# Performance work log

Hardware: AMD Instinct MI355X
Metric: run time of the kernel (lower is better)

Reference implementation:

```python
import jax, jax.numpy as jnp
import numpy as np
from jax import lax

HEADS = 8
DIM_HEAD = 64
INNER = HEADS * DIM_HEAD  # 512
LOG_SCALE_MAX = float(np.log(100.0))  # clamp for clamp_exp (SwinV2-style max temperature 1/0.01)
EPS_NORM = 1e-12  # F.normalize eps
EPS_LN = 1e-5


def setup_inputs() -> dict:
    key = jax.random.key(0)
    ks = jax.random.split(key, 6)
    b, c, h, w = 2, 256, 48, 48
    x = jax.random.normal(ks[0], (b, c, h, w), jnp.float32)
    w_in = jax.random.normal(ks[1], (3 * INNER, c), jnp.float32) * (c ** -0.5)
    b_in = jnp.zeros((3 * INNER,), jnp.float32)
    # learnable log-scale, init log(d_head ** -0.5), per head
    softmax_scale = jnp.full((HEADS, 1, 1), float(np.log(DIM_HEAD ** -0.5)), jnp.float32)
    w_dw = jax.random.normal(ks[2], (INNER, 1, 3, 3), jnp.float32) * (1.0 / 3.0)
    w_pw = jax.random.normal(ks[3], (2 * c, INNER), jnp.float32) * (INNER ** -0.5)
    gamma = jnp.full((2 * c,), 1e-3, jnp.float32)  # norm init_weight=0.001
    beta = jnp.zeros((2 * c,), jnp.float32)
    return {"x": x, "w_in": w_in, "b_in": b_in, "softmax_scale": softmax_scale,
            "w_dw": w_dw, "w_pw": w_pw, "gamma": gamma, "beta": beta}


def _l2norm(t):
    n = jnp.sqrt(jnp.sum(t * t, axis=-1, keepdims=True))
    return t / jnp.maximum(n, EPS_NORM)


def reference(x, w_in, b_in, softmax_scale, w_dw, w_pw, gamma, beta):
    b, c, h, w = x.shape
    s = h * w
    # proj_in: 1x1 conv then 'b (h c) x y -> b h x y c'
    y = jnp.einsum('bchw,oc->bohw', x, w_in) + b_in[None, :, None, None]
    y = y.reshape(b, HEADS, 3 * DIM_HEAD, h, w).transpose(0, 1, 3, 4, 2)  # b H x y (3*dh)
    y = y.reshape(b, HEADS, s, 3 * DIM_HEAD)
    q, k, v = jnp.split(y, 3, axis=-1)  # each [b, H, s, dh]
    # scaled cosine attention
    qn, kn = _l2norm(q), _l2norm(k)
    scale = jnp.exp(jnp.minimum(softmax_scale, LOG_SCALE_MAX))  # clamp_exp, [H,1,1]
    sim = jnp.einsum('bhid,bhjd->bhij', qn, kn) * scale[None]
    attn = jax.nn.softmax(sim, axis=-1)
    out = jnp.einsum('bhij,bhjd->bhid', attn, v)  # [b,H,s,dh]
    # unsplit heads -> 'b (h w) c' -> 'b c h w'
    update = out.transpose(0, 2, 1, 3).reshape(b, s, INNER)
    update = update.transpose(0, 2, 1).reshape(b, INNER, h, w)
    # proj_out: depthwise 3x3 (no bias) + pointwise 1x1 (no bias)
    dw = lax.conv_general_dilated(update, w_dw, (1, 1), 'SAME',
                                  feature_group_count=INNER,
                                  dimension_numbers=('NCHW', 'OIHW', 'NCHW'))
    pw = jnp.einsum('bchw,oc->bohw', dw, w_pw)  # [b, 2c, h, w]
    # channelwise layernorm with small init weight (norm_scales_and_shifts)
    mu = jnp.mean(pw, axis=1, keepdims=True)
    var = jnp.var(pw, axis=1, keepdims=True)
    normed = (pw - mu) * lax.rsqrt(var + EPS_LN)
    normed = normed * gamma[None, :, None, None] + beta[None, :, None, None]
    scales, shifts = jnp.split(normed, 2, axis=1)  # each [b, c, h, w]
    return shifts + x * scales
```

## Files before the change

### kernel.cpp

```cpp
#include <hip/hip_runtime.h>

#define B_ 2
#define C_ 256
#define S_ 2304
#define DH_ 64
#define O3_ 1536
#define INNER_ 512
#define LOGSMAX 4.605170185988092f
#define LOG2E 1.4426950408889634f

typedef __attribute__((ext_vector_type(8))) short short8;
typedef __attribute__((ext_vector_type(4))) float f32x4;
typedef __attribute__((ext_vector_type(16))) float f32x16;
typedef __attribute__((ext_vector_type(4))) unsigned short us4;
typedef __attribute__((ext_vector_type(2))) unsigned u32x2;
typedef __attribute__((ext_vector_type(4))) unsigned u32x4;
typedef __bf16 bf16x8 __attribute__((ext_vector_type(8)));

__device__ __forceinline__ unsigned short f2bf(float f) {
  unsigned u = __builtin_bit_cast(unsigned, f);
  u += 0x7FFFu + ((u >> 16) & 1u);
  return (unsigned short)(u >> 16);
}
__device__ __forceinline__ float bf2f(unsigned short h) {
  return __builtin_bit_cast(float, (unsigned)h << 16);
}
__device__ __forceinline__ bf16x8 as_bf(short8 v) {
  return __builtin_bit_cast(bf16x8, v);
}
__device__ __forceinline__ float fexp2(float x) {
#if __has_builtin(__builtin_amdgcn_exp2f)
  return __builtin_amdgcn_exp2f(x);
#else
  return __expf(x * 0.6931471805599453f);
#endif
}
__device__ __forceinline__ float frcp(float x) {
#if __has_builtin(__builtin_amdgcn_rcpf)
  return __builtin_amdgcn_rcpf(x);
#else
  return 1.f / x;
#endif
}
__device__ __forceinline__ unsigned pack_hi16(unsigned b, unsigned a) {
  return __builtin_amdgcn_perm(b, a, 0x07060302u);
}
__device__ __forceinline__ unsigned pack_lo16(unsigned b, unsigned a) {
  return __builtin_amdgcn_perm(b, a, 0x05040100u);
}

__global__ __launch_bounds__(256) void k_prep(const float* __restrict__ x,
                                              const float* __restrict__ w_in,
                                              const float* __restrict__ w_pw,
                                              unsigned short* __restrict__ xT,
                                              unsigned short* __restrict__ w_inb,
                                              unsigned short* __restrict__ w_pwb) {
  __shared__ float tile[64][65];
  int blk = blockIdx.x;
  int t = threadIdx.x;
  if (blk < 288) {
    int p0 = (blk % 36) * 64, c0 = ((blk / 36) % 4) * 64, b = blk / 144;
    const float* xb = x + (size_t)b * C_ * S_;
#pragma unroll
    for (int i = 0; i < 16; i++) {
      int c = i * 4 + (t >> 6);
      int p = t & 63;
      tile[c][p] = xb[(size_t)(c0 + c) * S_ + p0 + p];
    }
    __syncthreads();
    unsigned short* xTb = xT + (size_t)b * S_ * C_;
#pragma unroll
    for (int i = 0; i < 16; i++) {
      int p = i * 4 + (t >> 6);
      int c = t & 63;
      xTb[(size_t)(p0 + p) * C_ + c0 + c] = f2bf(tile[c][p]);
    }
  } else if (blk < 288 + 1536) {
    int i = (blk - 288) * 256 + t;
    w_inb[i] = f2bf(w_in[i]);
  } else {
    int i = (blk - 1824) * 256 + t;
    w_pwb[i] = f2bf(w_pw[i]);
  }
}

__global__ __launch_bounds__(256) void k_gemm_qkv(const unsigned short* __restrict__ A,
                                                  const unsigned short* __restrict__ BT,
                                                  const float* __restrict__ b_in,
                                                  const float* __restrict__ ss,
                                                  unsigned char* __restrict__ qn,
                                                  unsigned char* __restrict__ kn,
                                                  unsigned short* __restrict__ vv) {
  __shared__ __align__(16) unsigned short As[64][72];
  __shared__ __align__(16) unsigned short Bs[128][72];
  int t = threadIdx.x;
  int lane = t & 63, wv = t >> 6;
  int quad = lane >> 4, r15 = lane & 15;
  int by = blockIdx.y;
  int m0 = by * 64, n0 = blockIdx.x * 128;
  int b = blockIdx.z;
  const unsigned short* BTb = BT + (size_t)b * S_ * C_;

  f32x4 acc[4][2] = {};

  int srA = t >> 2, scA = (t & 3) * 16;
  int srB = t >> 1, scB = (t & 1) * 32;
  const unsigned short* ag = A + (size_t)(m0 + srA) * C_ + scA;
  const unsigned short* bg = BTb + (size_t)(n0 + srB) * C_ + scB;

  for (int k0 = 0; k0 < C_; k0 += 64) {
    short8 a0 = *(const short8*)(ag + k0);
    short8 a1 = *(const short8*)(ag + k0 + 8);
    short8 b0 = *(const short8*)(bg + k0);
    short8 b1 = *(const short8*)(bg + k0 + 8);
    short8 b2 = *(const short8*)(bg + k0 + 16);
    short8 b3 = *(const short8*)(bg + k0 + 24);
    __syncthreads();
    *(short8*)&As[srA][scA] = a0;
    *(short8*)&As[srA][scA + 8] = a1;
    *(short8*)&Bs[srB][scB] = b0;
    *(short8*)&Bs[srB][scB + 8] = b1;
    *(short8*)&Bs[srB][scB + 16] = b2;
    *(short8*)&Bs[srB][scB + 24] = b3;
    __syncthreads();
#pragma unroll
    for (int ks = 0; ks < 2; ks++) {
      short8 af[4], bfr[2];
#pragma unroll
      for (int i = 0; i < 4; i++) af[i] = *(const short8*)&As[i * 16 + r15][ks * 32 + quad * 8];
#pragma unroll
      for (int j = 0; j < 2; j++) bfr[j] = *(const short8*)&Bs[wv * 32 + j * 16 + r15][ks * 32 + quad * 8];
#pragma unroll
      for (int i = 0; i < 4; i++)
#pragma unroll
        for (int j = 0; j < 2; j++)
          acc[i][j] = __builtin_amdgcn_mfma_f32_16x16x32_bf16(as_bf(af[i]), as_bf(bfr[j]), acc[i][j], 0, 0, 0);
    }
  }

  int h = by / 3, seg = by - h * 3;
  int bh = b * 8 + h;
  f32x4 bi[4];
#pragma unroll
  for (int i = 0; i < 4; i++) bi[i] = *(const f32x4*)&b_in[m0 + i * 16 + quad * 4];
  float bv[4][2][4];
  float ssq0 = 0.f, ssq1 = 0.f;
#pragma unroll
  for (int i = 0; i < 4; i++)
#pragma unroll
    for (int rr = 0; rr < 4; rr++) {
      float v0 = acc[i][0][rr] + bi[i][rr];
      float v1 = acc[i][1][rr] + bi[i][rr];
      bv[i][0][rr] = v0;
      bv[i][1][rr] = v1;
      ssq0 += v0 * v0;
      ssq1 += v1 * v1;
    }
  if (seg < 2) {
    float sc = (seg == 0) ? __expf(fminf(ss[h], LOGSMAX)) * LOG2E : 1.f;
    ssq0 += __shfl_xor(ssq0, 16);
    ssq0 += __shfl_xor(ssq0, 32);
    ssq1 += __shfl_xor(ssq1, 16);
    ssq1 += __shfl_xor(ssq1, 32);
    float inv0 = sc / fmaxf(sqrtf(ssq0), 1e-12f);
    float inv1 = sc / fmaxf(sqrtf(ssq1), 1e-12f);
    unsigned char* dst = (seg == 0 ? qn : kn) + (size_t)bh * S_ * DH_;
#pragma unroll
    for (int i = 0; i < 4; i++)
#pragma unroll
      for (int j = 0; j < 2; j++) {
        float iv = j ? inv1 : inv0;
        int pk = __builtin_amdgcn_cvt_pk_fp8_f32(bv[i][j][0] * iv, bv[i][j][1] * iv, 0, false);
        pk = __builtin_amdgcn_cvt_pk_fp8_f32(bv[i][j][2] * iv, bv[i][j][3] * iv, pk, true);
        int p = n0 + wv * 32 + j * 16 + r15;
        *(int*)&dst[(size_t)p * DH_ + i * 16 + quad * 4] = pk;
      }
  } else {
    unsigned short* dst = vv + (size_t)bh * S_ * DH_;
#pragma unroll
    for (int i = 0; i < 4; i++)
#pragma unroll
      for (int j = 0; j < 2; j++) {
        us4 o = {f2bf(bv[i][j][0]), f2bf(bv[i][j][1]), f2bf(bv[i][j][2]), f2bf(bv[i][j][3])};
        int p = n0 + wv * 32 + j * 16 + r15;
        *(us4*)&dst[(size_t)p * DH_ + i * 16 + quad * 4] = o;
      }
  }
}

__global__ __launch_bounds__(128) void k_gemm2(const unsigned short* __restrict__ A,
                                               const unsigned short* __restrict__ BT,
                                               float* __restrict__ outp,
                                               int M, int N, int K) {
  __shared__ __align__(16) unsigned short As[64][72];
  __shared__ __align__(16) unsigned short Bs[64][72];
  int t = threadIdx.x;
  int lane = t & 63, wv = t >> 6;
  int quad = lane >> 4, r15 = lane & 15;
  int m0 = blockIdx.y * 64, n0 = blockIdx.x * 64;
  int b = blockIdx.z;
  const unsigned short* BTb = BT + (size_t)b * N * K;

  f32x4 acc[4][2] = {};

  int sr = t >> 1, sc = (t & 1) * 32;
  const unsigned short* ag = A + (size_t)(m0 + sr) * K + sc;
  const unsigned short* bg = BTb + (size_t)(n0 + sr) * K + sc;

  for (int k0 = 0; k0 < K; k0 += 64) {
    short8 a0 = *(const short8*)(ag + k0);
    short8 a1 = *(const short8*)(ag + k0 + 8);
    short8 a2 = *(const short8*)(ag + k0 + 16);
    short8 a3 = *(const short8*)(ag + k0 + 24);
    short8 b0 = *(const short8*)(bg + k0);
    short8 b1 = *(const short8*)(bg + k0 + 8);
    short8 b2 = *(const short8*)(bg + k0 + 16);
    short8 b3 = *(const short8*)(bg + k0 + 24);
    __syncthreads();
    *(short8*)&As[sr][sc] = a0;
    *(short8*)&As[sr][sc + 8] = a1;
    *(short8*)&As[sr][sc + 16] = a2;
    *(short8*)&As[sr][sc + 24] = a3;
    *(short8*)&Bs[sr][sc] = b0;
    *(short8*)&Bs[sr][sc + 8] = b1;
    *(short8*)&Bs[sr][sc + 16] = b2;
    *(short8*)&Bs[sr][sc + 24] = b3;
    __syncthreads();
#pragma unroll
    for (int ks = 0; ks < 2; ks++) {
      short8 af[4], bfr[2];
#pragma unroll
      for (int i = 0; i < 4; i++) af[i] = *(const short8*)&As[i * 16 + r15][ks * 32 + quad * 8];
#pragma unroll
      for (int j = 0; j < 2; j++) bfr[j] = *(const short8*)&Bs[wv * 32 + j * 16 + r15][ks * 32 + quad * 8];
#pragma unroll
      for (int i = 0; i < 4; i++)
#pragma unroll
        for (int j = 0; j < 2; j++)
          acc[i][j] = __builtin_amdgcn_mfma_f32_16x16x32_bf16(as_bf(af[i]), as_bf(bfr[j]), acc[i][j], 0, 0, 0);
    }
  }
  float* Cb = outp + (size_t)b * M * N;
#pragma unroll
  for (int i = 0; i < 4; i++)
#pragma unroll
    for (int j = 0; j < 2; j++)
#pragma unroll
      for (int rr = 0; rr < 4; rr++) {
        int row = m0 + i * 16 + quad * 4 + rr;
        int col = n0 + wv * 32 + j * 16 + r15;
        Cb[(size_t)row * N + col] = acc[i][j][rr];
      }
}

__global__ __launch_bounds__(256) void k_attn(const unsigned char* __restrict__ qn,
                                              const unsigned char* __restrict__ kn,
                                              const unsigned short* __restrict__ vv,
                                              const float* __restrict__ ss,
                                              unsigned short* __restrict__ attnp,
                                              float* __restrict__ lp) {
  __shared__ __align__(16) unsigned char Ks[64][72];
  __shared__ __align__(16) unsigned short Vs[64][72];
  __shared__ __align__(16) unsigned short Ps[4][32][76];
  int t = threadIdx.x;
  int w = t >> 6;
  int lane = t & 63;
  int l31 = lane & 31, hi = lane >> 5;
  int bh = blockIdx.x;
  int q0 = blockIdx.y * 128 + w * 32;
  int split = blockIdx.z;
  int ktbase = split * 12;
  const unsigned char* qb = qn + (size_t)bh * S_ * DH_;
  const unsigned char* kb = kn + (size_t)bh * S_ * DH_;
  const unsigned short* vb = vv + (size_t)bh * S_ * DH_;
  float shift2 = __expf(fminf(ss[bh & 7], LOGSMAX)) * LOG2E;

  const unsigned char* qrow = qb + (size_t)(q0 + l31) * DH_ + hi * 8;
  long qf[4];
#pragma unroll
  for (int ks = 0; ks < 4; ks++) qf[ks] = *(const long*)(qrow + ks * 16);

  const f32x16 z16 = {};
  f32x16 O0 = z16, O1 = z16;
  float l_part = 0.f;

  int srow = t >> 2;
  int scol = (t & 3) * 16;
  const unsigned char* kg = kb + ((size_t)(ktbase * 64) + srow) * DH_ + scol;

  int dp = w * 8 + ((t & 63) >> 3);
  int koct = t & 7;
  const unsigned* vg32 = (const unsigned*)vb + ((size_t)(ktbase * 64 + koct * 8)) * 32 + dp;

  uint4 kr = *(const uint4*)kg;
  unsigned lv[8];
#pragma unroll
  for (int kk = 0; kk < 8; kk++) lv[kk] = vg32[(size_t)kk * 32];

  for (int i = 0; i < 12; i++) {
    __syncthreads();
    *(uint4*)&Ks[srow][scol] = kr;
    {
      u32x4 ev = {pack_lo16(lv[1], lv[0]), pack_lo16(lv[3], lv[2]),
                  pack_lo16(lv[5], lv[4]), pack_lo16(lv[7], lv[6])};
      u32x4 od = {pack_hi16(lv[1], lv[0]), pack_hi16(lv[3], lv[2]),
                  pack_hi16(lv[5], lv[4]), pack_hi16(lv[7], lv[6])};
      *(u32x4*)&Vs[2 * dp][koct * 8] = ev;
      *(u32x4*)&Vs[2 * dp + 1][koct * 8] = od;
    }
    __syncthreads();
    if (i < 11) {
      kr = *(const uint4*)(kg + (size_t)(i + 1) * 64 * DH_);
      const unsigned* vg = vg32 + (size_t)(i + 1) * 64 * 32;
#pragma unroll
      for (int kk = 0; kk < 8; kk++) lv[kk] = vg[(size_t)kk * 32];
    }
    f32x16 sc0, sc1;
    {
      long a0 = *(const long*)&Ks[l31][hi * 8];
      long a1 = *(const long*)&Ks[32 + l31][hi * 8];
      sc0 = __builtin_amdgcn_mfma_f32_32x32x16_fp8_fp8(a0, qf[0], z16, 0, 0, 0);
      sc1 = __builtin_amdgcn_mfma_f32_32x32x16_fp8_fp8(a1, qf[0], z16, 0, 0, 0);
    }
#pragma unroll
    for (int ks = 1; ks < 4; ks++) {
      long a0 = *(const long*)&Ks[l31][ks * 16 + hi * 8];
      long a1 = *(const long*)&Ks[32 + l31][ks * 16 + hi * 8];
      sc0 = __builtin_amdgcn_mfma_f32_32x32x16_fp8_fp8(a0, qf[ks], sc0, 0, 0, 0);
      sc1 = __builtin_amdgcn_mfma_f32_32x32x16_fp8_fp8(a1, qf[ks], sc1, 0, 0, 0);
    }
    float lsum = 0.f;
#pragma unroll
    for (int mt = 0; mt < 2; mt++) {
      const f32x16& s = mt ? sc1 : sc0;
#pragma unroll
      for (int g = 0; g < 4; g++) {
        float e0 = fexp2(s[g * 4 + 0] - shift2);
        float e1 = fexp2(s[g * 4 + 1] - shift2);
        float e2 = fexp2(s[g * 4 + 2] - shift2);
        float e3 = fexp2(s[g * 4 + 3] - shift2);
        lsum += (e0 + e1) + (e2 + e3);
        unsigned u0 = __builtin_bit_cast(unsigned, e0) + 0x8000u;
        unsigned u1 = __builtin_bit_cast(unsigned, e1) + 0x8000u;
        unsigned u2 = __builtin_bit_cast(unsigned, e2) + 0x8000u;
        unsigned u3 = __builtin_bit_cast(unsigned, e3) + 0x8000u;
        u32x2 pk = {pack_hi16(u1, u0), pack_hi16(u3, u2)};
        *(u32x2*)&Ps[w][l31][mt * 32 + g * 8 + hi * 4] = pk;
      }
    }
    l_part += lsum;
#pragma unroll
    for (int ks = 0; ks < 4; ks++) {
      short8 pb = *(const short8*)&Ps[w][l31][ks * 16 + hi * 8];
      short8 va0 = *(const short8*)&Vs[l31][ks * 16 + hi * 8];
      short8 va1 = *(const short8*)&Vs[32 + l31][ks * 16 + hi * 8];
      O0 = __builtin_amdgcn_mfma_f32_32x32x16_bf16(as_bf(va0), as_bf(pb), O0, 0, 0, 0);
      O1 = __builtin_amdgcn_mfma_f32_32x32x16_bf16(as_bf(va1), as_bf(pb), O1, 0, 0, 0);
    }
  }
  float l = l_part + __shfl_xor(l_part, 32);
  if (hi == 0) lp[((size_t)(split * 16 + bh)) * S_ + q0 + l31] = l;
  unsigned short* orow = attnp + (((size_t)(split * 16 + bh)) * S_ + q0 + l31) * DH_;
#pragma unroll
  for (int mt = 0; mt < 2; mt++) {
    const f32x16& O = mt ? O1 : O0;
#pragma unroll
    for (int g = 0; g < 4; g++) {
      us4 o4 = {f2bf(O[g * 4 + 0]), f2bf(O[g * 4 + 1]), f2bf(O[g * 4 + 2]), f2bf(O[g * 4 + 3])};
      *(us4*)&orow[mt * 32 + g * 8 + hi * 4] = o4;
    }
  }
}

__global__ __launch_bounds__(256) void k_dwconv(const unsigned short* __restrict__ attnp,
                                                const float* __restrict__ lp,
                                                const float* __restrict__ w_dw,
                                                unsigned short* __restrict__ dwb) {
  int t = threadIdx.x;
  int d = t & 63;
  int pj = t >> 6;
  int p = blockIdx.y * 4 + pj;
  int bh = blockIdx.x;
  int b = bh >> 3, h = bh & 7;
  int yy = p / 48, xx = p % 48;
  const unsigned short* a0 = attnp + (size_t)bh * S_ * DH_ + d;
  const unsigned short* a1 = attnp + ((size_t)(16 + bh)) * S_ * DH_ + d;
  const unsigned short* a2 = attnp + ((size_t)(32 + bh)) * S_ * DH_ + d;
  const float* l0 = lp + (size_t)bh * S_;
  const float* l1 = lp + (size_t)(16 + bh) * S_;
  const float* l2 = lp + (size_t)(32 + bh) * S_;
  int ch = h * 64 + d;
  float w[9];
#pragma unroll
  for (int i = 0; i < 9; i++) w[i] = w_dw[ch * 9 + i];
  float acc = 0.f;
#pragma unroll
  for (int dy = -1; dy <= 1; dy++) {
    int y2 = yy + dy;
    if (y2 < 0 || y2 >= 48) continue;
#pragma unroll
    for (int dx = -1; dx <= 1; dx++) {
      int x2 = xx + dx;
      if (x2 < 0 || x2 >= 48) continue;
      int p2 = y2 * 48 + x2;
      float rl = frcp(l0[p2] + l1[p2] + l2[p2]);
      float v = (bf2f(a0[(size_t)p2 * DH_]) + bf2f(a1[(size_t)p2 * DH_]) + bf2f(a2[(size_t)p2 * DH_])) * rl;
      acc += v * w[(dy + 1) * 3 + dx + 1];
    }
  }
  dwb[((size_t)b * S_ + p) * INNER_ + ch] = f2bf(acc);
}

__global__ __launch_bounds__(256) void k_ln_final(const float* __restrict__ pw,
                                                  const float* __restrict__ gamma,
                                                  const float* __restrict__ beta,
                                                  const float* __restrict__ x,
                                                  float* __restrict__ out) {
  __shared__ float s_s0[32][8], s_s1[32][8], s_q0[32][8], s_q1[32][8];
  int t = threadIdx.x;
  int pl = t & 7, g = t >> 3;
  int b = blockIdx.y;
  int p = blockIdx.x * 16 + pl * 2;
  const float* pwb = pw + (size_t)b * INNER_ * S_ + p;
  float s0 = 0.f, s1 = 0.f, q0 = 0.f, q1 = 0.f;
#pragma unroll
  for (int j = 0; j < 16; j++) {
    float2 v = *(const float2*)&pwb[(size_t)(g * 16 + j) * S_];
    s0 += v.x; s1 += v.y;
    q0 += v.x * v.x; q1 += v.y * v.y;
  }
  s_s0[g][pl] = s0; s_s1[g][pl] = s1;
  s_q0[g][pl] = q0; s_q1[g][pl] = q1;
  __syncthreads();
  float t0 = 0.f, t1 = 0.f, u0 = 0.f, u1 = 0.f;
#pragma unroll
  for (int i = 0; i < 32; i++) {
    t0 += s_s0[i][pl]; t1 += s_s1[i][pl];
    u0 += s_q0[i][pl]; u1 += s_q1[i][pl];
  }
  float mu0 = t0 * (1.f / 512.f), mu1 = t1 * (1.f / 512.f);
  float rs0 = rsqrtf(u0 * (1.f / 512.f) - mu0 * mu0 + 1e-5f);
  float rs1 = rsqrtf(u1 * (1.f / 512.f) - mu1 * mu1 + 1e-5f);
  const float* xb = x + (size_t)b * C_ * S_ + p;
  float* ob = out + (size_t)b * C_ * S_ + p;
#pragma unroll
  for (int j = 0; j < 8; j++) {
    int cc = g * 8 + j;
    float ga = gamma[cc], be = beta[cc];
    float gs = gamma[cc + 256], bs = beta[cc + 256];
    float2 pv = *(const float2*)&pwb[(size_t)cc * S_];
    float2 sv = *(const float2*)&pwb[(size_t)(cc + 256) * S_];
    float2 xv = *(const float2*)&xb[(size_t)cc * S_];
    float sc0 = (pv.x - mu0) * rs0 * ga + be;
    float sc1 = (pv.y - mu1) * rs1 * ga + be;
    float sh0 = (sv.x - mu0) * rs0 * gs + bs;
    float sh1 = (sv.y - mu1) * rs1 * gs + bs;
    float2 o;
    o.x = sh0 + xv.x * sc0;
    o.y = sh1 + xv.y * sc1;
    *(float2*)&ob[(size_t)cc * S_] = o;
  }
}

extern "C" void kernel_launch(void* const* d_in, const int* in_sizes, int n_in,
                              void* d_out, int out_size, void* d_ws, size_t ws_size,
                              hipStream_t stream) {
  const float* x = (const float*)d_in[0];
  const float* w_in = (const float*)d_in[1];
  const float* b_in = (const float*)d_in[2];
  const float* ss = (const float*)d_in[3];
  const float* w_dw = (const float*)d_in[4];
  const float* w_pw = (const float*)d_in[5];
  const float* gamma = (const float*)d_in[6];
  const float* beta = (const float*)d_in[7];
  float* out = (float*)d_out;
  char* ws = (char*)d_ws;

  unsigned short* xT = (unsigned short*)(ws + 0);
  unsigned short* w_inb = (unsigned short*)(ws + 2359296);
  unsigned short* w_pwb = (unsigned short*)(ws + 3145728);
  unsigned char* qn = (unsigned char*)(ws + 3670016);
  unsigned char* kn = (unsigned char*)(ws + 6029312);
  unsigned short* vv = (unsigned short*)(ws + 8388608);
  unsigned short* dwb = (unsigned short*)(ws + 13107200);
  float* lp = (float*)(ws + 17825792);
  unsigned short* attnp = (unsigned short*)(ws + 18268160);
  float* pw = (float*)(ws + 32423936);

  k_prep<<<2848, 256, 0, stream>>>(x, w_in, w_pw, xT, w_inb, w_pwb);
  k_gemm_qkv<<<dim3(18, 24, 2), 256, 0, stream>>>(w_inb, xT, b_in, ss, qn, kn, vv);
  k_attn<<<dim3(16, 18, 3), 256, 0, stream>>>(qn, kn, vv, ss, attnp, lp);
  k_dwconv<<<dim3(16, 576), 256, 0, stream>>>(attnp, lp, w_dw, dwb);
  k_gemm2<<<dim3(36, 8, 2), 128, 0, stream>>>(w_pwb, dwb, pw, INNER_, S_, INNER_);
  k_ln_final<<<dim3(144, 2), 256, 0, stream>>>(pw, gamma, beta, x, out);
}
```

Baseline: 165.7 us.

## Split attention KV into four chunks and pass P via cross-lane shuffles

The attention kernel now splits the 36 key tiles across 4 z-splits of 9 tiles instead of 3 of 12, which gives 1152 blocks and better occupancy across CUs. The dwconv combine stage reads and sums four partials, and the workspace offsets are shifted to make room. In a separate change, the bf16 probability tile no longer goes through LDS: the MFMA B-operand is built in registers with __shfl_xor across half-waves, which removes the Ps writes and reads. The cost is more partial-output traffic and extra shuffle instructions.

```diff
diff --git a/kernel.cpp b/kernel.cpp
--- a/kernel.cpp
+++ b/kernel.cpp
@@ -47,6 +47,11 @@
 }
 __device__ __forceinline__ unsigned pack_lo16(unsigned b, unsigned a) {
   return __builtin_amdgcn_perm(b, a, 0x05040100u);
+}
+__device__ __forceinline__ unsigned pk2(float a, float b) {
+  unsigned ua = __builtin_bit_cast(unsigned, a) + 0x8000u;
+  unsigned ub = __builtin_bit_cast(unsigned, b) + 0x8000u;
+  return pack_hi16(ub, ua);
 }
 
 __global__ __launch_bounds__(256) void k_prep(const float* __restrict__ x,
@@ -261,7 +266,6 @@
                                               float* __restrict__ lp) {
   __shared__ __align__(16) unsigned char Ks[64][72];
   __shared__ __align__(16) unsigned short Vs[64][72];
-  __shared__ __align__(16) unsigned short Ps[4][32][76];
   int t = threadIdx.x;
   int w = t >> 6;
   int lane = t & 63;
@@ -269,7 +273,7 @@
   int bh = blockIdx.x;
   int q0 = blockIdx.y * 128 + w * 32;
   int split = blockIdx.z;
-  int ktbase = split * 12;
+  int ktbase = split * 9;
   const unsigned char* qb = qn + (size_t)bh * S_ * DH_;
   const unsigned char* kb = kn + (size_t)bh * S_ * DH_;
   const unsigned short* vb = vv + (size_t)bh * S_ * DH_;
@@ -297,7 +301,7 @@
 #pragma unroll
   for (int kk = 0; kk < 8; kk++) lv[kk] = vg32[(size_t)kk * 32];
 
-  for (int i = 0; i < 12; i++) {
+  for (int i = 0; i < 9; i++) {
     __syncthreads();
     *(uint4*)&Ks[srow][scol] = kr;
     {
@@ -309,7 +313,7 @@
       *(u32x4*)&Vs[2 * dp + 1][koct * 8] = od;
     }
     __syncthreads();
-    if (i < 11) {
+    if (i < 8) {
       kr = *(const uint4*)(kg + (size_t)(i + 1) * 64 * DH_);
       const unsigned* vg = vg32 + (size_t)(i + 1) * 64 * 32;
 #pragma unroll
@@ -329,33 +333,41 @@
       sc0 = __builtin_amdgcn_mfma_f32_32x32x16_fp8_fp8(a0, qf[ks], sc0, 0, 0, 0);
       sc1 = __builtin_amdgcn_mfma_f32_32x32x16_fp8_fp8(a1, qf[ks], sc1, 0, 0, 0);
     }
-    float lsum = 0.f;
 #pragma unroll
     for (int mt = 0; mt < 2; mt++) {
       const f32x16& s = mt ? sc1 : sc0;
-#pragma unroll
-      for (int g = 0; g < 4; g++) {
-        float e0 = fexp2(s[g * 4 + 0] - shift2);
-        float e1 = fexp2(s[g * 4 + 1] - shift2);
-        float e2 = fexp2(s[g * 4 + 2] - shift2);
-        float e3 = fexp2(s[g * 4 + 3] - shift2);
+      unsigned pk[8];
+      float lsum = 0.f;
+#pragma unroll
+      for (int g2 = 0; g2 < 4; g2++) {
+        float e0 = fexp2(s[g2 * 4 + 0] - shift2);
+        float e1 = fexp2(s[g2 * 4 + 1] - shift2);
+        float e2 = fexp2(s[g2 * 4 + 2] - shift2);
+        float e3 = fexp2(s[g2 * 4 + 3] - shift2);
         lsum += (e0 + e1) + (e2 + e3);
-        unsigned u0 = __builtin_bit_cast(unsigned, e0) + 0x8000u;
-        unsigned u1 = __builtin_bit_cast(unsigned, e1) + 0x8000u;
-        unsigned u2 = __builtin_bit_cast(unsigned, e2) + 0x8000u;
-        unsigned u3 = __builtin_bit_cast(unsigned, e3) + 0x8000u;
-        u32x2 pk = {pack_hi16(u1, u0), pack_hi16(u3, u2)};
-        *(u32x2*)&Ps[w][l31][mt * 32 + g * 8 + hi * 4] = pk;
+        pk[2 * g2] = pk2(e0, e1);
+        pk[2 * g2 + 1] = pk2(e2, e3);
       }
-    }
-    l_part += lsum;
-#pragma unroll
-    for (int ks = 0; ks < 4; ks++) {
-      short8 pb = *(const short8*)&Ps[w][l31][ks * 16 + hi * 8];
-      short8 va0 = *(const short8*)&Vs[l31][ks * 16 + hi * 8];
-      short8 va1 = *(const short8*)&Vs[32 + l31][ks * 16 + hi * 8];
-      O0 = __builtin_amdgcn_mfma_f32_32x32x16_bf16(as_bf(va0), as_bf(pb), O0, 0, 0, 0);
-      O1 = __builtin_amdgcn_mfma_f32_32x32x16_bf16(as_bf(va1), as_bf(pb), O1, 0, 0, 0);
+      l_part += lsum;
+#pragma unroll
+      for (int half = 0; half < 2; half++) {
+        int gb = half * 4;
+        unsigned ya = hi ? pk[gb + 0] : pk[gb + 2];
+        unsigned yb = hi ? pk[gb + 1] : pk[gb + 3];
+        unsigned ra = __shfl_xor(ya, 32);
+        unsigned rb = __shfl_xor(yb, 32);
+        u32x4 fd;
+        fd[0] = hi ? ra : pk[gb + 0];
+        fd[1] = hi ? rb : pk[gb + 1];
+        fd[2] = hi ? pk[gb + 2] : ra;
+        fd[3] = hi ? pk[gb + 3] : rb;
+        short8 pb = __builtin_bit_cast(short8, fd);
+        int ks = mt * 2 + half;
+        short8 va0 = *(const short8*)&Vs[l31][ks * 16 + hi * 8];
+        short8 va1 = *(const short8*)&Vs[32 + l31][ks * 16 + hi * 8];
+        O0 = __builtin_amdgcn_mfma_f32_32x32x16_bf16(as_bf(va0), as_bf(pb), O0, 0, 0, 0);
+        O1 = __builtin_amdgcn_mfma_f32_32x32x16_bf16(as_bf(va1), as_bf(pb), O1, 0, 0, 0);
+      }
     }
   }
   float l = l_part + __shfl_xor(l_part, 32);
@@ -386,9 +398,11 @@
   const unsigned short* a0 = attnp + (size_t)bh * S_ * DH_ + d;
   const unsigned short* a1 = attnp + ((size_t)(16 + bh)) * S_ * DH_ + d;
   const unsigned short* a2 = attnp + ((size_t)(32 + bh)) * S_ * DH_ + d;
+  const unsigned short* a3 = attnp + ((size_t)(48 + bh)) * S_ * DH_ + d;
   const float* l0 = lp + (size_t)bh * S_;
   const float* l1 = lp + (size_t)(16 + bh) * S_;
   const float* l2 = lp + (size_t)(32 + bh) * S_;
+  const float* l3 = lp + (size_t)(48 + bh) * S_;
   int ch = h * 64 + d;
   float w[9];
 #pragma unroll
@@ -403,8 +417,9 @@
       int x2 = xx + dx;
       if (x2 < 0 || x2 >= 48) continue;
       int p2 = y2 * 48 + x2;
-      float rl = frcp(l0[p2] + l1[p2] + l2[p2]);
-      float v = (bf2f(a0[(size_t)p2 * DH_]) + bf2f(a1[(size_t)p2 * DH_]) + bf2f(a2[(size_t)p2 * DH_])) * rl;
+      float rl = frcp(l0[p2] + l1[p2] + l2[p2] + l3[p2]);
+      float v = (bf2f(a0[(size_t)p2 * DH_]) + bf2f(a1[(size_t)p2 * DH_]) +
+                 bf2f(a2[(size_t)p2 * DH_]) + bf2f(a3[(size_t)p2 * DH_])) * rl;
       acc += v * w[(dy + 1) * 3 + dx + 1];
     }
   }
@@ -484,12 +499,12 @@
   unsigned short* vv = (unsigned short*)(ws + 8388608);
   unsigned short* dwb = (unsigned short*)(ws + 13107200);
   float* lp = (float*)(ws + 17825792);
-  unsigned short* attnp = (unsigned short*)(ws + 18268160);
-  float* pw = (float*)(ws + 32423936);
+  unsigned short* attnp = (unsigned short*)(ws + 18415616);
+  float* pw = (float*)(ws + 37289984);
 
   k_prep<<<2848, 256, 0, stream>>>(x, w_in, w_pw, xT, w_inb, w_pwb);
   k_gemm_qkv<<<dim3(18, 24, 2), 256, 0, stream>>>(w_inb, xT, b_in, ss, qn, kn, vv);
-  k_attn<<<dim3(16, 18, 3), 256, 0, stream>>>(qn, kn, vv, ss, attnp, lp);
+  k_attn<<<dim3(16, 18, 4), 256, 0, stream>>>(qn, kn, vv, ss, attnp, lp);
   k_dwconv<<<dim3(16, 576), 256, 0, stream>>>(attnp, lp, w_dw, dwb);
   k_gemm2<<<dim3(36, 8, 2), 128, 0, stream>>>(w_pwb, dwb, pw, INNER_, S_, INNER_);
   k_ln_final<<<dim3(144, 2), 256, 0, stream>>>(pw, gamma, beta, x, out);
```

After: 166.6 us. Within noise of the previous version (+0.5%).
